# Optimization experiments

Measured on AMD Instinct MI355X. Metric: run time of the kernel, lower is better.

## Reference

```python
import jax, jax.numpy as jnp
import numpy as np

BETA = 0.9  # leaky-integrator decay of the stateful neuron


def setup_inputs() -> dict:
    key = jax.random.key(0)
    k = jax.random.split(key, 5)
    B, T, I, H, O = 128, 512, 1024, 2048, 512
    x = jax.random.normal(k[0], (B, T, I), dtype=jnp.float32)
    # Linear params, PyTorch-style scaling
    W_in = jax.random.normal(k[1], (I, H), dtype=jnp.float32) / np.sqrt(I)
    b_in = jax.random.normal(k[2], (H,), dtype=jnp.float32) / np.sqrt(I)
    W_out = jax.random.normal(k[3], (H, O), dtype=jnp.float32) / np.sqrt(H)
    b_out = jax.random.normal(k[4], (O,), dtype=jnp.float32) / np.sqrt(H)
    return {"x": x, "W_in": W_in, "b_in": b_in, "W_out": W_out, "b_out": b_out}


def reference(x, W_in, b_in, W_out, b_out):
    # x: [B, T, I]
    B, T, _ = x.shape
    # fc_in applied to every timestep at once (same math as per-step Linear)
    h = jnp.einsum('bti,ih->bth', x, W_in) + b_in  # [B, T, H]

    # stateful neuron: leaky integration s_t = BETA * s_{t-1} + h_t, via scan
    def step(s, h_t):
        s = BETA * s + h_t
        return s, s

    s0 = jnp.zeros((B, h.shape[-1]), dtype=h.dtype)
    _, S = jax.lax.scan(step, s0, jnp.swapaxes(h, 0, 1))  # S: [T, B, H]

    # readout per timestep, then reduce over time (readout_mode='sum')
    logits = jnp.einsum('tbh,ho->tbo', S, W_out) + b_out  # [T, B, O]
    return logits.sum(axis=0)  # [B, O]
```

## Files before the change

### kernel.cpp

```cpp
#include <hip/hip_runtime.h>
#include <hip/hip_bf16.h>
#include <math.h>

constexpr int B_ = 128, T_ = 512, I_ = 1024, H_ = 2048, O_ = 512;
#define BETA 0.9f

constexpr int WOFF = 0;
constexpr int YOFF = 512;
constexpr int ZOFF = YOFF + B_ * I_;
constexpr int WS_FLOATS = ZOFF + B_ * H_;

typedef __attribute__((ext_vector_type(4))) short short4v;
typedef __attribute__((ext_vector_type(8))) short short8v;
typedef __attribute__((ext_vector_type(4))) float float4v;

__global__ __launch_bounds__(256) void init_kernel(float* __restrict__ ws,
                                                   const float* __restrict__ b_in,
                                                   const float* __restrict__ b_out,
                                                   float* __restrict__ out, float wsum) {
    int idx = blockIdx.x * 256 + threadIdx.x;
    const int total = WS_FLOATS + B_ * O_;
    if (idx >= total) return;
    if (idx < 512) {
        ws[idx] = (1.0f - powf(BETA, (float)(T_ - idx))) * (1.0f / (1.0f - BETA));
    } else if (idx < ZOFF) {
        ws[idx] = 0.0f;
    } else if (idx < WS_FLOATS) {
        int j = idx - ZOFF;
        ws[idx] = wsum * b_in[j & (H_ - 1)];
    } else {
        int j = idx - WS_FLOATS;
        out[j] = (float)T_ * b_out[j & (O_ - 1)];
    }
}

constexpr int TCH = 128;
__global__ __launch_bounds__(256) void wreduce_kernel(const float* __restrict__ x,
                                                      float* __restrict__ ws) {
    __shared__ float wl[TCH];
    const int b  = blockIdx.x >> 2;
    const int tc = blockIdx.x & 3;
    const int t0 = tc * TCH;
    if (threadIdx.x < TCH) wl[threadIdx.x] = ws[WOFF + t0 + threadIdx.x];
    __syncthreads();

    const int i = threadIdx.x * 4;
    const float* xp = x + (size_t)b * T_ * I_ + (size_t)t0 * I_ + i;
    float4v acc = {0.f, 0.f, 0.f, 0.f};
#pragma unroll 4
    for (int tb = 0; tb < TCH; tb += 8) {
        float4v v[8];
#pragma unroll
        for (int j = 0; j < 8; ++j)
            v[j] = __builtin_nontemporal_load((const float4v*)(xp + (size_t)(tb + j) * I_));
#pragma unroll
        for (int j = 0; j < 8; ++j) {
            const float wt = wl[tb + j];
            acc.x += wt * v[j].x; acc.y += wt * v[j].y;
            acc.z += wt * v[j].z; acc.w += wt * v[j].w;
        }
    }
    float* yp = ws + YOFF + b * I_ + i;
    atomicAdd(yp + 0, acc.x);
    atomicAdd(yp + 1, acc.y);
    atomicAdd(yp + 2, acc.z);
    atomicAdd(yp + 3, acc.w);
}

template <int KGLOB, int NGLOB, int KCH>
__global__ __launch_bounds__(256) void mm128(const float* __restrict__ A,
                                             const float* __restrict__ Bm,
                                             float* __restrict__ C) {
    constexpr int BN = 64, BK = 32, PAD = 8;
    __shared__ __align__(16) __hip_bfloat16 As[128][BK + PAD];
    __shared__ __align__(16) __hip_bfloat16 Bs[BN][BK + PAD];

    const int n0    = blockIdx.x * BN;
    const int kbase = blockIdx.y * KCH;
    const int tid   = threadIdx.x;
    const int lane  = tid & 63;
    const int w     = tid >> 6;
    const int lo    = lane & 15;
    const int hi    = lane >> 4;

    float4v acc[2][4];
#pragma unroll
    for (int mf = 0; mf < 2; ++mf)
#pragma unroll
        for (int nf = 0; nf < 4; ++nf) acc[mf][nf] = (float4v){0.f, 0.f, 0.f, 0.f};

    for (int k0 = kbase; k0 < kbase + KCH; k0 += BK) {
        {
            const int row = tid >> 1;
            const int kh  = (tid & 1) * 16;
            const float* ap = A + (size_t)row * KGLOB + k0 + kh;
#pragma unroll
            for (int j = 0; j < 4; ++j) {
                float4 v = *(const float4*)(ap + 4 * j);
                union { short4v s; __hip_bfloat16 h[4]; } u;
                u.h[0] = __float2bfloat16(v.x); u.h[1] = __float2bfloat16(v.y);
                u.h[2] = __float2bfloat16(v.z); u.h[3] = __float2bfloat16(v.w);
                *(short4v*)&As[row][kh + 4 * j] = u.s;
            }
        }
        {
            const int k  = tid >> 3;
            const int nq = (tid & 7) * 8;
            const float* bp = Bm + (size_t)(k0 + k) * NGLOB + n0 + nq;
#pragma unroll
            for (int j = 0; j < 2; ++j) {
                float4 v = *(const float4*)(bp + 4 * j);
                Bs[nq + 4 * j + 0][k] = __float2bfloat16(v.x);
                Bs[nq + 4 * j + 1][k] = __float2bfloat16(v.y);
                Bs[nq + 4 * j + 2][k] = __float2bfloat16(v.z);
                Bs[nq + 4 * j + 3][k] = __float2bfloat16(v.w);
            }
        }
        __syncthreads();
        {
            const int kk = hi * 8;
            short8v a[2], bv[4];
#pragma unroll
            for (int mf = 0; mf < 2; ++mf)
                a[mf] = *(const short8v*)&As[w * 32 + mf * 16 + lo][kk];
#pragma unroll
            for (int nf = 0; nf < 4; ++nf)
                bv[nf] = *(const short8v*)&Bs[nf * 16 + lo][kk];
#pragma unroll
            for (int mf = 0; mf < 2; ++mf)
#pragma unroll
                for (int nf = 0; nf < 4; ++nf)
                    acc[mf][nf] = __builtin_amdgcn_mfma_f32_16x16x32_bf16(
                        a[mf], bv[nf], acc[mf][nf], 0, 0, 0);
        }
        __syncthreads();
    }
#pragma unroll
    for (int mf = 0; mf < 2; ++mf)
#pragma unroll
        for (int nf = 0; nf < 4; ++nf)
#pragma unroll
            for (int i = 0; i < 4; ++i) {
                const int row = w * 32 + mf * 16 + hi * 4 + i;
                const int col = n0 + nf * 16 + lo;
                atomicAdd(&C[(size_t)row * NGLOB + col], acc[mf][nf][i]);
            }
}

extern "C" void kernel_launch(void* const* d_in, const int* in_sizes, int n_in,
                              void* d_out, int out_size, void* d_ws, size_t ws_size,
                              hipStream_t stream) {
    const float* x     = (const float*)d_in[0];
    const float* W_in  = (const float*)d_in[1];
    const float* b_in  = (const float*)d_in[2];
    const float* W_out = (const float*)d_in[3];
    const float* b_out = (const float*)d_in[4];
    float* out = (float*)d_out;
    float* ws  = (float*)d_ws;

    const double beta = 0.9;
    const double bT = pow(beta, (double)T_);
    const float wsum = (float)(((double)T_ - beta * (1.0 - bT) / (1.0 - beta)) / (1.0 - beta));

    const int total = WS_FLOATS + B_ * O_;
    init_kernel<<<(total + 255) / 256, 256, 0, stream>>>(ws, b_in, b_out, out, wsum);

    wreduce_kernel<<<B_ * (T_ / TCH), 256, 0, stream>>>(x, ws);

    mm128<I_, H_, 128><<<dim3(H_ / 64, I_ / 128), 256, 0, stream>>>(ws + YOFF, W_in, ws + ZOFF);

    mm128<H_, O_, 64><<<dim3(O_ / 64, H_ / 64), 256, 0, stream>>>(ws + ZOFF, W_out, out);
}
```

Measured before the change: 76.25 us.

## Split time rows across waves in wreduce with LDS cross-wave reduction

The weighted time-reduction kernel now gives each wavefront its own 32-timestep slice, and each lane covers four columns strided by 256 floats. That replaces one thread per four columns walking all 128 timesteps. Partial sums are combined through a shared-memory reduction across the four waves before the atomic adds. Nontemporal loads are dropped in favour of plain vector loads. The aim is more independent memory streams per wave and better latency hiding on the dominant 256MB read of x, at the cost of extra LDS use and a block barrier.

```diff
diff --git a/kernel.cpp b/kernel.cpp
--- a/kernel.cpp
+++ b/kernel.cpp
@@ -38,33 +38,50 @@
 __global__ __launch_bounds__(256) void wreduce_kernel(const float* __restrict__ x,
                                                       float* __restrict__ ws) {
     __shared__ float wl[TCH];
+    __shared__ __align__(16) float red[4 * 256 * 4];
     const int b  = blockIdx.x >> 2;
     const int tc = blockIdx.x & 3;
     const int t0 = tc * TCH;
     if (threadIdx.x < TCH) wl[threadIdx.x] = ws[WOFF + t0 + threadIdx.x];
     __syncthreads();
 
-    const int i = threadIdx.x * 4;
-    const float* xp = x + (size_t)b * T_ * I_ + (size_t)t0 * I_ + i;
-    float4v acc = {0.f, 0.f, 0.f, 0.f};
+    const int w = threadIdx.x >> 6;
+    const int l = threadIdx.x & 63;
+    const float* xb = x + (size_t)b * T_ * I_ + (size_t)(t0 + w * 32) * I_ + l * 4;
+
+    float4v acc0 = {0,0,0,0}, acc1 = {0,0,0,0}, acc2 = {0,0,0,0}, acc3 = {0,0,0,0};
 #pragma unroll 4
-    for (int tb = 0; tb < TCH; tb += 8) {
+    for (int tt = 0; tt < 32; tt += 2) {
+        const float* r0 = xb + (size_t)tt * I_;
         float4v v[8];
 #pragma unroll
-        for (int j = 0; j < 8; ++j)
-            v[j] = __builtin_nontemporal_load((const float4v*)(xp + (size_t)(tb + j) * I_));
+        for (int j = 0; j < 4; ++j) v[j]     = *(const float4v*)(r0 + j * 256);
 #pragma unroll
-        for (int j = 0; j < 8; ++j) {
-            const float wt = wl[tb + j];
-            acc.x += wt * v[j].x; acc.y += wt * v[j].y;
-            acc.z += wt * v[j].z; acc.w += wt * v[j].w;
-        }
+        for (int j = 0; j < 4; ++j) v[4 + j] = *(const float4v*)(r0 + I_ + j * 256);
+        const float w0 = wl[w * 32 + tt], w1 = wl[w * 32 + tt + 1];
+        acc0 += w0 * v[0] + w1 * v[4];
+        acc1 += w0 * v[1] + w1 * v[5];
+        acc2 += w0 * v[2] + w1 * v[6];
+        acc3 += w0 * v[3] + w1 * v[7];
     }
-    float* yp = ws + YOFF + b * I_ + i;
-    atomicAdd(yp + 0, acc.x);
-    atomicAdd(yp + 1, acc.y);
-    atomicAdd(yp + 2, acc.z);
-    atomicAdd(yp + 3, acc.w);
+    *(float4v*)&red[(w * 256 + 0 * 64 + l) * 4] = acc0;
+    *(float4v*)&red[(w * 256 + 1 * 64 + l) * 4] = acc1;
+    *(float4v*)&red[(w * 256 + 2 * 64 + l) * 4] = acc2;
+    *(float4v*)&red[(w * 256 + 3 * 64 + l) * 4] = acc3;
+    __syncthreads();
+    {
+        const int s = threadIdx.x;
+        float4v r = *(const float4v*)&red[(0 * 256 + s) * 4]
+                  + *(const float4v*)&red[(1 * 256 + s) * 4]
+                  + *(const float4v*)&red[(2 * 256 + s) * 4]
+                  + *(const float4v*)&red[(3 * 256 + s) * 4];
+        const int i = (s >> 6) * 256 + (s & 63) * 4;
+        float* yp = ws + YOFF + (size_t)b * I_ + i;
+        atomicAdd(yp + 0, r.x);
+        atomicAdd(yp + 1, r.y);
+        atomicAdd(yp + 2, r.z);
+        atomicAdd(yp + 3, r.w);
+    }
 }
 
 template <int KGLOB, int NGLOB, int KCH>
```

After: 75.11 us. About the same (-1.5%).
